# Kernel tuning notes

Measured on AMD Instinct MI355X. Metric: run time of the kernel, lower is better.

The kernel has to match this reference:

```python
import jax, jax.numpy as jnp
import numpy as np

N = 100000   # nodes
E = 6400000  # edges (avg degree 64)
F = 512      # num_features
C = 16       # num_classes

def _glorot(key, shape):
    fan_in, fan_out = shape
    lim = (6.0 / (fan_in + fan_out)) ** 0.5
    return jax.random.uniform(key, shape, jnp.float32, -lim, lim)

def setup_inputs() -> dict:
    key = jax.random.key(0)
    ks = jax.random.split(key, 8)
    x = jax.random.normal(ks[0], (N, F), jnp.float32)
    edge_index = jax.random.randint(ks[1], (2, E), 0, N, dtype=jnp.int64)
    return {
        "x": x,
        "edge_index": edge_index,
        "W1": _glorot(ks[2], (F, 16)), "b1": jnp.zeros((16,), jnp.float32),
        "W2": _glorot(ks[3], (16, 32)), "b2": jnp.zeros((32,), jnp.float32),
        "W3": _glorot(ks[4], (32, C)),  "b3": jnp.zeros((C,), jnp.float32),
        "Wc": _glorot(ks[5], (C, C)),   "bc": jnp.zeros((C,), jnp.float32),
    }

def _gcn_conv(x, row, col, norm, W, b):
    # PyG GCNConv: transform, then normalized sum-aggregation, then bias
    h = x @ W                                   # [N, out]
    msg = h[row] * norm[:, None]                # gather + scale, [E+N, out]
    agg = jax.ops.segment_sum(msg, col, num_segments=N)
    return agg + b

def reference(x, edge_index, W1, b1, W2, b2, W3, b3, Wc, bc):
    n = x.shape[0]
    loops = jnp.arange(n, dtype=edge_index.dtype)
    row = jnp.concatenate([edge_index[0], loops])  # source
    col = jnp.concatenate([edge_index[1], loops])  # target
    # symmetric normalization D^{-1/2} A_hat D^{-1/2}
    deg = jax.ops.segment_sum(jnp.ones_like(col, dtype=x.dtype), col, num_segments=n)
    dis = jnp.where(deg > 0, jax.lax.rsqrt(deg), 0.0)
    norm = dis[row] * dis[col]                     # [E+N]
    h = jax.nn.relu(_gcn_conv(x, row, col, norm, W1, b1))
    h = jax.nn.relu(_gcn_conv(h, row, col, norm, W2, b2))
    h = jax.nn.relu(_gcn_conv(h, row, col, norm, W3, b3))
    out = h @ Wc + bc
    return (out, h)
```

## Files before the change

### kernel.cpp

```cpp
#include <hip/hip_runtime.h>
#include <hip/hip_bf16.h>
#include <hip/hip_fp16.h>
#include <stdint.h>


#define MS_CHUNK 15360

__device__ __forceinline__ int blockScanExclusive256(int v, int* wsum) {
  int lane = threadIdx.x & 63;
  int wid  = threadIdx.x >> 6;
  int inc = v;
#pragma unroll
  for (int d = 1; d < 64; d <<= 1) {
    int y = __shfl_up(inc, d, 64);
    if (lane >= d) inc += y;
  }
  if (lane == 63) wsum[wid] = inc;
  __syncthreads();
  if (threadIdx.x == 0) {
    int s = 0;
#pragma unroll
    for (int w = 0; w < 4; ++w) { int t = wsum[w]; wsum[w] = s; s += t; }
  }
  __syncthreads();
  return inc - v + wsum[wid];
}

__device__ __forceinline__ int blockScanExclusive512(int v, int* wsum) {
  int lane = threadIdx.x & 63;
  int wid  = threadIdx.x >> 6;
  int inc = v;
#pragma unroll
  for (int d = 1; d < 64; d <<= 1) {
    int y = __shfl_up(inc, d, 64);
    if (lane >= d) inc += y;
  }
  if (lane == 63) wsum[wid] = inc;
  __syncthreads();
  if (threadIdx.x == 0) {
    int s = 0;
#pragma unroll
    for (int w = 0; w < 8; ++w) { int t = wsum[w]; wsum[w] = s; s += t; }
  }
  __syncthreads();
  return inc - v + wsum[wid];
}

__global__ __launch_bounds__(256) void k_bhist(const int* __restrict__ ecol,
                                               int* __restrict__ cntmat,
                                               int e, int chunk, int nb) {
  __shared__ int h[256];
  h[threadIdx.x] = 0;
  __syncthreads();
  int g = blockIdx.x;
  int s0 = g * chunk;
  int s1 = min(e, s0 + chunk);
  int i = s0 + threadIdx.x;
  for (; i + 768 < s1; i += 1024) {
    int c0 = ecol[i], c1 = ecol[i + 256], c2 = ecol[i + 512], c3 = ecol[i + 768];
    atomicAdd(&h[c0 >> 9], 1);
    atomicAdd(&h[c1 >> 9], 1);
    atomicAdd(&h[c2 >> 9], 1);
    atomicAdd(&h[c3 >> 9], 1);
  }
  for (; i < s1; i += 256) atomicAdd(&h[ecol[i] >> 9], 1);
  __syncthreads();
  for (int b = threadIdx.x; b < nb; b += 256) cntmat[g * nb + b] = h[b];
}

__global__ __launch_bounds__(256) void k_colscan(int* __restrict__ cntmat,
                                                 int* __restrict__ colsum,
                                                 int G, int nb) {
  __shared__ int wsum[4];
  __shared__ int carry_s;
  int b = blockIdx.x;
  if (threadIdx.x == 0) carry_s = 0;
  __syncthreads();
  for (int base = 0; base < G; base += 256) {
    int i = base + threadIdx.x;
    int v = (i < G) ? cntmat[i * nb + b] : 0;
    int ex = blockScanExclusive256(v, wsum);
    int c = carry_s;
    __syncthreads();
    if (i < G) cntmat[i * nb + b] = ex + c;
    if (threadIdx.x == 255) carry_s = c + ex + v;
    __syncthreads();
  }
  if (threadIdx.x == 0) colsum[b] = carry_s;
}

__global__ __launch_bounds__(256) void k_bscan(const int* __restrict__ colsum,
                                               int* __restrict__ bbase,
                                               int nb, int etot) {
  __shared__ int wsum[4];
  __shared__ int carry_s;
  if (threadIdx.x == 0) carry_s = 0;
  __syncthreads();
  for (int base = 0; base < nb; base += 256) {
    int i = base + threadIdx.x;
    int v = (i < nb) ? colsum[i] : 0;
    int ex = blockScanExclusive256(v, wsum);
    int c = carry_s;
    __syncthreads();
    if (i < nb) bbase[i] = ex + c;
    if (threadIdx.x == 255) carry_s = c + ex + v;
    __syncthreads();
  }
  if (threadIdx.x == 0) bbase[nb] = etot;
}

__global__ __launch_bounds__(256) void k_scatter_ms(
    const int* __restrict__ erow, const int* __restrict__ ecol,
    const int* __restrict__ cntmat, const int* __restrict__ colsum,
    const int* __restrict__ bbase, unsigned* __restrict__ sorted,
    int e, int chunk, int nb, int G) {
  __shared__ unsigned staging[MS_CHUNK];
  __shared__ int lstart[256];
  __shared__ int lfill[256];
  __shared__ int gbase[256];
  __shared__ int wsum[4];
  int g = blockIdx.x;
  for (int b = threadIdx.x; b < nb; b += 256) {
    int cur = cntmat[g * nb + b];
    int nxt = (g + 1 < G) ? cntmat[(g + 1) * nb + b] : colsum[b];
    lfill[b] = nxt - cur;
    gbase[b] = bbase[b] + cur;
  }
  __syncthreads();
  int v = (threadIdx.x < nb) ? lfill[threadIdx.x] : 0;
  int ex = blockScanExclusive256(v, wsum);
  if (threadIdx.x < nb) lstart[threadIdx.x] = ex;
  __syncthreads();
  if (threadIdx.x < nb) lfill[threadIdx.x] = 0;
  __syncthreads();
  int s0 = g * chunk;
  int s1 = min(e, s0 + chunk);
  int i = s0 + threadIdx.x;
  for (; i + 768 < s1; i += 1024) {
    int c0 = ecol[i],       c1 = ecol[i + 256], c2 = ecol[i + 512], c3 = ecol[i + 768];
    int r0 = erow[i],       r1 = erow[i + 256], r2 = erow[i + 512], r3 = erow[i + 768];
    int b0 = c0 >> 9, b1 = c1 >> 9, b2 = c2 >> 9, b3 = c3 >> 9;
    int p0 = atomicAdd(&lfill[b0], 1);
    int p1 = atomicAdd(&lfill[b1], 1);
    int p2 = atomicAdd(&lfill[b2], 1);
    int p3 = atomicAdd(&lfill[b3], 1);
    staging[lstart[b0] + p0] = ((unsigned)r0 << 9) | (unsigned)(c0 & 511);
    staging[lstart[b1] + p1] = ((unsigned)r1 << 9) | (unsigned)(c1 & 511);
    staging[lstart[b2] + p2] = ((unsigned)r2 << 9) | (unsigned)(c2 & 511);
    staging[lstart[b3] + p3] = ((unsigned)r3 << 9) | (unsigned)(c3 & 511);
  }
  for (; i < s1; i += 256) {
    int c = ecol[i];
    int b = c >> 9;
    int p = atomicAdd(&lfill[b], 1);
    staging[lstart[b] + p] = ((unsigned)erow[i] << 9) | (unsigned)(c & 511);
  }
  __syncthreads();
  int wid = threadIdx.x >> 6, L = threadIdx.x & 63;
  for (int b = wid; b < nb; b += 4) {
    int len = lfill[b];
    int ls = lstart[b], gb = gbase[b];
    for (int j = L; j < len; j += 64)
      sorted[gb + j] = staging[ls + j];
  }
}

__global__ __launch_bounds__(256) void k_transform1(
    const float* __restrict__ x, const float* __restrict__ W,
    __half* __restrict__ t1raw, int n) {
  int L = threadIdx.x & 63;
  int wid = blockIdx.x * 4 + (threadIdx.x >> 6);
  int nw = gridDim.x * 4;

  float w[8][16];
  const float4* W4 = reinterpret_cast<const float4*>(W);
#pragma unroll
  for (int i = 0; i < 4; ++i) {
#pragma unroll
    for (int c4 = 0; c4 < 4; ++c4) {
      float4 va = W4[(4 * L + i) * 4 + c4];
      w[i][c4 * 4 + 0] = va.x; w[i][c4 * 4 + 1] = va.y;
      w[i][c4 * 4 + 2] = va.z; w[i][c4 * 4 + 3] = va.w;
      float4 vb = W4[(256 + 4 * L + i) * 4 + c4];
      w[4 + i][c4 * 4 + 0] = vb.x; w[4 + i][c4 * 4 + 1] = vb.y;
      w[4 + i][c4 * 4 + 2] = vb.z; w[4 + i][c4 * 4 + 3] = vb.w;
    }
  }
  int col = ((L & 1) << 3) | ((L & 2) << 1) | ((L & 4) >> 1) | ((L & 8) >> 3);

  for (int r = wid; r < n; r += nw) {
    const float4* xr = reinterpret_cast<const float4*>(x + (size_t)r * 512);
    float4 v0 = xr[L];
    float4 v1 = xr[64 + L];
    float acc[16];
#pragma unroll
    for (int c = 0; c < 16; ++c) {
      float a = v0.x * w[0][c];
      a = fmaf(v0.y, w[1][c], a);
      a = fmaf(v0.z, w[2][c], a);
      a = fmaf(v0.w, w[3][c], a);
      a = fmaf(v1.x, w[4][c], a);
      a = fmaf(v1.y, w[5][c], a);
      a = fmaf(v1.z, w[6][c], a);
      a = fmaf(v1.w, w[7][c], a);
      acc[c] = a;
    }
#pragma unroll
    for (int j = 0; j < 8; ++j) {
      float send = (L & 1) ? acc[j] : acc[j + 8];
      float recv = __shfl_xor(send, 1, 64);
      acc[j] = ((L & 1) ? acc[j + 8] : acc[j]) + recv;
    }
#pragma unroll
    for (int j = 0; j < 4; ++j) {
      float send = (L & 2) ? acc[j] : acc[j + 4];
      float recv = __shfl_xor(send, 2, 64);
      acc[j] = ((L & 2) ? acc[j + 4] : acc[j]) + recv;
    }
#pragma unroll
    for (int j = 0; j < 2; ++j) {
      float send = (L & 4) ? acc[j] : acc[j + 2];
      float recv = __shfl_xor(send, 4, 64);
      acc[j] = ((L & 4) ? acc[j + 2] : acc[j]) + recv;
    }
    {
      float send = (L & 8) ? acc[0] : acc[1];
      float recv = __shfl_xor(send, 8, 64);
      acc[0] = ((L & 8) ? acc[1] : acc[0]) + recv;
    }
    float s = acc[0];
    s += __shfl_xor(s, 16, 64);
    s += __shfl_xor(s, 32, 64);
    if (L < 16) t1raw[r * 16 + col] = __float2half(s);
  }
}

__global__ __launch_bounds__(512) void k_pass2(const unsigned* __restrict__ sorted,
                                               const int* __restrict__ bbase,
                                               float* __restrict__ dis,
                                               int* __restrict__ rowptr,
                                               __half* __restrict__ t1,
                                               int* __restrict__ csr,
                                               int n, int etot) {
  __shared__ int hist[512];
  __shared__ int cur[512];
  __shared__ int wsum[8];
  int b = blockIdx.x;
  hist[threadIdx.x] = 0;
  __syncthreads();
  int s0 = bbase[b], s1 = bbase[b + 1];
  for (int i = s0 + threadIdx.x; i < s1; i += 512)
    atomicAdd(&hist[sorted[i] & 511], 1);
  __syncthreads();
  int j = threadIdx.x;
  int node = (b << 9) + j;
  int deg = hist[j];
  int ex = blockScanExclusive512(deg, wsum);
  float dv = rsqrtf((float)(deg + 1));
  cur[j] = s0 + ex;
  if (node < n) {
    dis[node] = dv;
    rowptr[node] = s0 + ex;
    __half2* t2 = reinterpret_cast<__half2*>(t1 + ((size_t)node << 4));
#pragma unroll
    for (int q = 0; q < 8; ++q) {
      float2 fv = __half22float2(t2[q]);
      fv.x *= dv; fv.y *= dv;
      t2[q] = __float22half2_rn(fv);
    }
  }
  if (b == 0 && threadIdx.x == 0) rowptr[n] = etot;
  __syncthreads();
  for (int i = s0 + threadIdx.x; i < s1; i += 512) {
    unsigned v = sorted[i];
    int pos = atomicAdd(&cur[v & 511], 1);
    csr[pos] = (int)(v >> 9);
  }
}

__device__ __forceinline__ float gather16(const __half* __restrict__ hs,
                                          const int* __restrict__ rowptr,
                                          const int* __restrict__ csr,
                                          int node, int f) {
  float acc0 = __half2float(hs[(node << 4) + f]);
  int e0 = rowptr[node], e1 = rowptr[node + 1];
  int e = e0;
  float acc1 = 0.f, acc2 = 0.f, acc3 = 0.f;
  for (; e + 16 <= e1; e += 16) {
    int r0  = csr[e + 0],  r1  = csr[e + 1],  r2  = csr[e + 2],  r3  = csr[e + 3];
    int r4  = csr[e + 4],  r5  = csr[e + 5],  r6  = csr[e + 6],  r7  = csr[e + 7];
    int r8  = csr[e + 8],  r9  = csr[e + 9],  r10 = csr[e + 10], r11 = csr[e + 11];
    int r12 = csr[e + 12], r13 = csr[e + 13], r14 = csr[e + 14], r15 = csr[e + 15];
    __half v0  = hs[(r0  << 4) + f], v1  = hs[(r1  << 4) + f];
    __half v2  = hs[(r2  << 4) + f], v3  = hs[(r3  << 4) + f];
    __half v4  = hs[(r4  << 4) + f], v5  = hs[(r5  << 4) + f];
    __half v6  = hs[(r6  << 4) + f], v7  = hs[(r7  << 4) + f];
    __half v8  = hs[(r8  << 4) + f], v9  = hs[(r9  << 4) + f];
    __half v10 = hs[(r10 << 4) + f], v11 = hs[(r11 << 4) + f];
    __half v12 = hs[(r12 << 4) + f], v13 = hs[(r13 << 4) + f];
    __half v14 = hs[(r14 << 4) + f], v15 = hs[(r15 << 4) + f];
    acc0 += (__half2float(v0)  + __half2float(v1))  + (__half2float(v2)  + __half2float(v3));
    acc1 += (__half2float(v4)  + __half2float(v5))  + (__half2float(v6)  + __half2float(v7));
    acc2 += (__half2float(v8)  + __half2float(v9))  + (__half2float(v10) + __half2float(v11));
    acc3 += (__half2float(v12) + __half2float(v13)) + (__half2float(v14) + __half2float(v15));
  }
  for (; e + 4 <= e1; e += 4) {
    int r0 = csr[e + 0], r1 = csr[e + 1], r2 = csr[e + 2], r3 = csr[e + 3];
    float v0 = __half2float(hs[(r0 << 4) + f]), v1 = __half2float(hs[(r1 << 4) + f]);
    float v2 = __half2float(hs[(r2 << 4) + f]), v3 = __half2float(hs[(r3 << 4) + f]);
    acc0 += (v0 + v1) + (v2 + v3);
  }
  for (; e < e1; ++e) acc0 += __half2float(hs[(csr[e] << 4) + f]);
  return (acc0 + acc1) + (acc2 + acc3);
}

__global__ __launch_bounds__(256) void k_agg_rb(
    const __half* __restrict__ hs, const int* __restrict__ rowptr,
    const int* __restrict__ csr, const float* __restrict__ dis,
    const float* __restrict__ b, __half* __restrict__ out, int n) {
  int node = blockIdx.x * 16 + threadIdx.x / 16;
  int f = threadIdx.x % 16;
  if (node >= n) return;
  float acc = gather16(hs, rowptr, csr, node, f);
  float d = dis[node];
  float t = fmaxf(fmaf(d, acc, b[f]), 0.f);
  out[(node << 4) + f] = __float2half(t * d);
}

__global__ __launch_bounds__(256) void k_agg_mid(
    const __half* __restrict__ hs, const int* __restrict__ rowptr,
    const int* __restrict__ csr, const float* __restrict__ dis,
    const float* __restrict__ W2, const float* __restrict__ b2,
    const float* __restrict__ W3, __half* __restrict__ out, int n) {
  __shared__ float w2s[512];
  __shared__ float w3s[512];
  __shared__ float b2s[32];
  for (int i = threadIdx.x; i < 512; i += 256) { w2s[i] = W2[i]; w3s[i] = W3[i]; }
  if (threadIdx.x < 32) b2s[threadIdx.x] = b2[threadIdx.x];
  __syncthreads();
  int node = blockIdx.x * 16 + threadIdx.x / 16;
  int f = threadIdx.x % 16;
  if (node >= n) return;
  float acc = gather16(hs, rowptr, csr, node, f);
  float d = dis[node];
  float v = d * acc;
  int base = threadIdx.x & 48;
  float a0 = b2s[f], a1 = b2s[f + 16];
#pragma unroll
  for (int k = 0; k < 16; ++k) {
    float vk = __shfl(v, base + k, 64);
    a0 = fmaf(vk, w2s[k * 32 + f], a0);
    a1 = fmaf(vk, w2s[k * 32 + 16 + f], a1);
  }
  a0 = fmaxf(a0, 0.f);
  a1 = fmaxf(a1, 0.f);
  float t = 0.f;
#pragma unroll
  for (int c = 0; c < 16; ++c) {
    float h0 = __shfl(a0, base + c, 64);
    float h1 = __shfl(a1, base + c, 64);
    t = fmaf(h0, w3s[c * 16 + f], t);
    t = fmaf(h1, w3s[(c + 16) * 16 + f], t);
  }
  out[(node << 4) + f] = __float2half(t * d);
}

__global__ __launch_bounds__(256) void k_agg_out(
    const __half* __restrict__ hs, const int* __restrict__ rowptr,
    const int* __restrict__ csr, const float* __restrict__ dis,
    const float* __restrict__ b3, const float* __restrict__ Wc,
    const float* __restrict__ bc, float* __restrict__ outh,
    float* __restrict__ outc, int n) {
  __shared__ float wcs[256];
  __shared__ float b3s[16];
  __shared__ float bcs[16];
  if (threadIdx.x < 256) wcs[threadIdx.x] = Wc[threadIdx.x];
  if (threadIdx.x < 16) { b3s[threadIdx.x] = b3[threadIdx.x]; bcs[threadIdx.x] = bc[threadIdx.x]; }
  __syncthreads();
  int node = blockIdx.x * 16 + threadIdx.x / 16;
  int f = threadIdx.x % 16;
  if (node >= n) return;
  float acc = gather16(hs, rowptr, csr, node, f);
  float d = dis[node];
  float h = fmaxf(fmaf(d, acc, b3s[f]), 0.f);
  outh[(node << 4) + f] = h;
  int base = threadIdx.x & 48;
  float o = bcs[f];
#pragma unroll
  for (int k = 0; k < 16; ++k) {
    float hk = __shfl(h, base + k, 64);
    o = fmaf(hk, wcs[k * 16 + f], o);
  }
  outc[(node << 4) + f] = o;
}

extern "C" void kernel_launch(void* const* d_in, const int* in_sizes, int n_in,
                              void* d_out, int out_size, void* d_ws, size_t ws_size,
                              hipStream_t stream) {
  (void)n_in; (void)out_size;
  const float* x  = (const float*)d_in[0];
  const int*   ei = (const int*)d_in[1];
  const float* W1 = (const float*)d_in[2];
  const float* b1 = (const float*)d_in[3];
  const float* W2 = (const float*)d_in[4];
  const float* b2 = (const float*)d_in[5];
  const float* W3 = (const float*)d_in[6];
  const float* b3 = (const float*)d_in[7];
  const float* Wc = (const float*)d_in[8];
  const float* bc = (const float*)d_in[9];

  const int F = 512;
  int N = in_sizes[0] / F;
  int E = in_sizes[1] / 2;
  const int* erow = ei;
  const int* ecol = ei + E;
  int NB = (N + 511) >> 9;
  const int chunk = MS_CHUNK;
  int GS = (E + chunk - 1) / chunk;

  auto align = [](size_t v) { return (v + 255) & ~(size_t)255; };
  char* p = (char*)d_ws;
  int*   cntmat = (int*)p;   p += align((size_t)GS * NB * 4);
  int*   colsum = (int*)p;   p += align(256 * 4);
  int*   bbase  = (int*)p;   p += align(257 * 4);
  float* dis    = (float*)p; p += align((size_t)N * 4);
  int*   rowptr = (int*)p;   p += align(((size_t)N + 1) * 4);
  int*   csr    = (int*)p;   p += align((size_t)E * 4);
  unsigned* sorted = (unsigned*)p; p += align((size_t)E * 4);
  __half* bufA = (__half*)p; p += align((size_t)N * 16 * 2);
  __half* bufB = (__half*)p; p += align((size_t)N * 16 * 2);
  if ((size_t)(p - (char*)d_ws) > ws_size) return;

  float* outc = (float*)d_out;
  float* outh = (float*)d_out + (size_t)N * 16;

  k_bhist<<<GS, 256, 0, stream>>>(ecol, cntmat, E, chunk, NB);
  k_colscan<<<NB, 256, 0, stream>>>(cntmat, colsum, GS, NB);
  k_bscan<<<1, 256, 0, stream>>>(colsum, bbase, NB, E);
  k_scatter_ms<<<GS, 256, 0, stream>>>(erow, ecol, cntmat, colsum, bbase,
                                       sorted, E, chunk, NB, GS);
  k_transform1<<<2048, 256, 0, stream>>>(x, W1, bufA, N);
  k_pass2<<<NB, 512, 0, stream>>>(sorted, bbase, dis, rowptr, bufA, csr, N, E);

  k_agg_rb<<<(N + 15) / 16, 256, 0, stream>>>(bufA, rowptr, csr, dis, b1, bufB, N);
  k_agg_mid<<<(N + 15) / 16, 256, 0, stream>>>(bufB, rowptr, csr, dis, W2, b2, W3, bufA, N);
  k_agg_out<<<(N + 15) / 16, 256, 0, stream>>>(bufA, rowptr, csr, dis, b3, Wc, bc, outh, outc, N);
}
```

Measured before the change: 311.8 us.

## Replace multi-pass bucket sort with atomic-cursor fixed-capacity bucket scatter

Drops the separate histogram, column-scan and global-offset kernels and instead has each scatter block count its own bucket sizes, then claim space in fixed-capacity per-bucket regions through global atomic cursors. The cursors are zeroed inside the transform kernel, and the bucket prefix scan moves after the scatter. It also loads the CSR neighbour indices once per 16-lane group and distributes them with wave shuffles instead of having every lane load all 16. Bucket order across blocks becomes nondeterministic, and correctness relies on no bucket exceeding the fixed capacity, which holds only for roughly uniform edge distributions.

```diff
diff --git a/kernel.cpp b/kernel.cpp
--- a/kernel.cpp
+++ b/kernel.cpp
@@ -46,50 +46,7 @@
   return inc - v + wsum[wid];
 }
 
-__global__ __launch_bounds__(256) void k_bhist(const int* __restrict__ ecol,
-                                               int* __restrict__ cntmat,
-                                               int e, int chunk, int nb) {
-  __shared__ int h[256];
-  h[threadIdx.x] = 0;
-  __syncthreads();
-  int g = blockIdx.x;
-  int s0 = g * chunk;
-  int s1 = min(e, s0 + chunk);
-  int i = s0 + threadIdx.x;
-  for (; i + 768 < s1; i += 1024) {
-    int c0 = ecol[i], c1 = ecol[i + 256], c2 = ecol[i + 512], c3 = ecol[i + 768];
-    atomicAdd(&h[c0 >> 9], 1);
-    atomicAdd(&h[c1 >> 9], 1);
-    atomicAdd(&h[c2 >> 9], 1);
-    atomicAdd(&h[c3 >> 9], 1);
-  }
-  for (; i < s1; i += 256) atomicAdd(&h[ecol[i] >> 9], 1);
-  __syncthreads();
-  for (int b = threadIdx.x; b < nb; b += 256) cntmat[g * nb + b] = h[b];
-}
-
-__global__ __launch_bounds__(256) void k_colscan(int* __restrict__ cntmat,
-                                                 int* __restrict__ colsum,
-                                                 int G, int nb) {
-  __shared__ int wsum[4];
-  __shared__ int carry_s;
-  int b = blockIdx.x;
-  if (threadIdx.x == 0) carry_s = 0;
-  __syncthreads();
-  for (int base = 0; base < G; base += 256) {
-    int i = base + threadIdx.x;
-    int v = (i < G) ? cntmat[i * nb + b] : 0;
-    int ex = blockScanExclusive256(v, wsum);
-    int c = carry_s;
-    __syncthreads();
-    if (i < G) cntmat[i * nb + b] = ex + c;
-    if (threadIdx.x == 255) carry_s = c + ex + v;
-    __syncthreads();
-  }
-  if (threadIdx.x == 0) colsum[b] = carry_s;
-}
-
-__global__ __launch_bounds__(256) void k_bscan(const int* __restrict__ colsum,
+__global__ __launch_bounds__(256) void k_bscan(const int* __restrict__ counts,
                                                int* __restrict__ bbase,
                                                int nb, int etot) {
   __shared__ int wsum[4];
@@ -98,7 +55,7 @@
   __syncthreads();
   for (int base = 0; base < nb; base += 256) {
     int i = base + threadIdx.x;
-    int v = (i < nb) ? colsum[i] : 0;
+    int v = (i < nb) ? counts[i] : 0;
     int ex = blockScanExclusive256(v, wsum);
     int c = carry_s;
     __syncthreads();
@@ -109,65 +66,79 @@
   if (threadIdx.x == 0) bbase[nb] = etot;
 }
 
-__global__ __launch_bounds__(256) void k_scatter_ms(
+__global__ __launch_bounds__(256) void k_scatter1(
     const int* __restrict__ erow, const int* __restrict__ ecol,
-    const int* __restrict__ cntmat, const int* __restrict__ colsum,
-    const int* __restrict__ bbase, unsigned* __restrict__ sorted,
-    int e, int chunk, int nb, int G) {
+    int* __restrict__ cursor, unsigned* __restrict__ sorted,
+    int e, int chunk, int nb, int cap) {
   __shared__ unsigned staging[MS_CHUNK];
   __shared__ int lstart[256];
   __shared__ int lfill[256];
   __shared__ int gbase[256];
   __shared__ int wsum[4];
   int g = blockIdx.x;
-  for (int b = threadIdx.x; b < nb; b += 256) {
-    int cur = cntmat[g * nb + b];
-    int nxt = (g + 1 < G) ? cntmat[(g + 1) * nb + b] : colsum[b];
-    lfill[b] = nxt - cur;
-    gbase[b] = bbase[b] + cur;
-  }
-  __syncthreads();
-  int v = (threadIdx.x < nb) ? lfill[threadIdx.x] : 0;
-  int ex = blockScanExclusive256(v, wsum);
-  if (threadIdx.x < nb) lstart[threadIdx.x] = ex;
-  __syncthreads();
-  if (threadIdx.x < nb) lfill[threadIdx.x] = 0;
-  __syncthreads();
   int s0 = g * chunk;
   int s1 = min(e, s0 + chunk);
-  int i = s0 + threadIdx.x;
-  for (; i + 768 < s1; i += 1024) {
-    int c0 = ecol[i],       c1 = ecol[i + 256], c2 = ecol[i + 512], c3 = ecol[i + 768];
-    int r0 = erow[i],       r1 = erow[i + 256], r2 = erow[i + 512], r3 = erow[i + 768];
-    int b0 = c0 >> 9, b1 = c1 >> 9, b2 = c2 >> 9, b3 = c3 >> 9;
-    int p0 = atomicAdd(&lfill[b0], 1);
-    int p1 = atomicAdd(&lfill[b1], 1);
-    int p2 = atomicAdd(&lfill[b2], 1);
-    int p3 = atomicAdd(&lfill[b3], 1);
-    staging[lstart[b0] + p0] = ((unsigned)r0 << 9) | (unsigned)(c0 & 511);
-    staging[lstart[b1] + p1] = ((unsigned)r1 << 9) | (unsigned)(c1 & 511);
-    staging[lstart[b2] + p2] = ((unsigned)r2 << 9) | (unsigned)(c2 & 511);
-    staging[lstart[b3] + p3] = ((unsigned)r3 << 9) | (unsigned)(c3 & 511);
-  }
-  for (; i < s1; i += 256) {
-    int c = ecol[i];
-    int b = c >> 9;
-    int p = atomicAdd(&lfill[b], 1);
-    staging[lstart[b] + p] = ((unsigned)erow[i] << 9) | (unsigned)(c & 511);
+  lfill[threadIdx.x] = 0;
+  __syncthreads();
+  {
+    int i = s0 + threadIdx.x;
+    for (; i + 768 < s1; i += 1024) {
+      int c0 = ecol[i], c1 = ecol[i + 256], c2 = ecol[i + 512], c3 = ecol[i + 768];
+      atomicAdd(&lfill[c0 >> 9], 1);
+      atomicAdd(&lfill[c1 >> 9], 1);
+      atomicAdd(&lfill[c2 >> 9], 1);
+      atomicAdd(&lfill[c3 >> 9], 1);
+    }
+    for (; i < s1; i += 256) atomicAdd(&lfill[ecol[i] >> 9], 1);
+  }
+  __syncthreads();
+  int cnt = lfill[threadIdx.x];
+  int ex = blockScanExclusive256(cnt, wsum);
+  lstart[threadIdx.x] = ex;
+  int gb = 0;
+  if (threadIdx.x < nb && cnt > 0) gb = atomicAdd(&cursor[threadIdx.x], cnt);
+  gbase[threadIdx.x] = gb;
+  __syncthreads();
+  lfill[threadIdx.x] = 0;
+  __syncthreads();
+  {
+    int i = s0 + threadIdx.x;
+    for (; i + 768 < s1; i += 1024) {
+      int c0 = ecol[i],       c1 = ecol[i + 256], c2 = ecol[i + 512], c3 = ecol[i + 768];
+      int r0 = erow[i],       r1 = erow[i + 256], r2 = erow[i + 512], r3 = erow[i + 768];
+      int b0 = c0 >> 9, b1 = c1 >> 9, b2 = c2 >> 9, b3 = c3 >> 9;
+      int p0 = atomicAdd(&lfill[b0], 1);
+      int p1 = atomicAdd(&lfill[b1], 1);
+      int p2 = atomicAdd(&lfill[b2], 1);
+      int p3 = atomicAdd(&lfill[b3], 1);
+      staging[lstart[b0] + p0] = ((unsigned)r0 << 9) | (unsigned)(c0 & 511);
+      staging[lstart[b1] + p1] = ((unsigned)r1 << 9) | (unsigned)(c1 & 511);
+      staging[lstart[b2] + p2] = ((unsigned)r2 << 9) | (unsigned)(c2 & 511);
+      staging[lstart[b3] + p3] = ((unsigned)r3 << 9) | (unsigned)(c3 & 511);
+    }
+    for (; i < s1; i += 256) {
+      int c = ecol[i];
+      int b = c >> 9;
+      int p = atomicAdd(&lfill[b], 1);
+      staging[lstart[b] + p] = ((unsigned)erow[i] << 9) | (unsigned)(c & 511);
+    }
   }
   __syncthreads();
   int wid = threadIdx.x >> 6, L = threadIdx.x & 63;
   for (int b = wid; b < nb; b += 4) {
     int len = lfill[b];
-    int ls = lstart[b], gb = gbase[b];
+    int ls = lstart[b];
+    int gdst = b * cap + gbase[b];
     for (int j = L; j < len; j += 64)
-      sorted[gb + j] = staging[ls + j];
+      sorted[gdst + j] = staging[ls + j];
   }
 }
 
 __global__ __launch_bounds__(256) void k_transform1(
     const float* __restrict__ x, const float* __restrict__ W,
-    __half* __restrict__ t1raw, int n) {
+    __half* __restrict__ t1raw, int* __restrict__ cursor, int n) {
+  if (blockIdx.x == 0) cursor[threadIdx.x] = 0;
+
   int L = threadIdx.x & 63;
   int wid = blockIdx.x * 4 + (threadIdx.x >> 6);
   int nw = gridDim.x * 4;
@@ -236,19 +207,21 @@
 }
 
 __global__ __launch_bounds__(512) void k_pass2(const unsigned* __restrict__ sorted,
+                                               const int* __restrict__ counts,
                                                const int* __restrict__ bbase,
                                                float* __restrict__ dis,
                                                int* __restrict__ rowptr,
                                                __half* __restrict__ t1,
                                                int* __restrict__ csr,
-                                               int n, int etot) {
+                                               int n, int etot, int cap) {
   __shared__ int hist[512];
   __shared__ int cur[512];
   __shared__ int wsum[8];
   int b = blockIdx.x;
   hist[threadIdx.x] = 0;
   __syncthreads();
-  int s0 = bbase[b], s1 = bbase[b + 1];
+  int s0 = b * cap;
+  int s1 = s0 + counts[b];
   for (int i = s0 + threadIdx.x; i < s1; i += 512)
     atomicAdd(&hist[sorted[i] & 511], 1);
   __syncthreads();
@@ -257,10 +230,11 @@
   int deg = hist[j];
   int ex = blockScanExclusive512(deg, wsum);
   float dv = rsqrtf((float)(deg + 1));
-  cur[j] = s0 + ex;
+  int gpos = bbase[b] + ex;
+  cur[j] = gpos;
   if (node < n) {
     dis[node] = dv;
-    rowptr[node] = s0 + ex;
+    rowptr[node] = gpos;
     __half2* t2 = reinterpret_cast<__half2*>(t1 + ((size_t)node << 4));
 #pragma unroll
     for (int q = 0; q < 8; ++q) {
@@ -282,15 +256,21 @@
                                           const int* __restrict__ rowptr,
                                           const int* __restrict__ csr,
                                           int node, int f) {
+  int base = (int)(threadIdx.x & 48);
   float acc0 = __half2float(hs[(node << 4) + f]);
   int e0 = rowptr[node], e1 = rowptr[node + 1];
   int e = e0;
   float acc1 = 0.f, acc2 = 0.f, acc3 = 0.f;
   for (; e + 16 <= e1; e += 16) {
-    int r0  = csr[e + 0],  r1  = csr[e + 1],  r2  = csr[e + 2],  r3  = csr[e + 3];
-    int r4  = csr[e + 4],  r5  = csr[e + 5],  r6  = csr[e + 6],  r7  = csr[e + 7];
-    int r8  = csr[e + 8],  r9  = csr[e + 9],  r10 = csr[e + 10], r11 = csr[e + 11];
-    int r12 = csr[e + 12], r13 = csr[e + 13], r14 = csr[e + 14], r15 = csr[e + 15];
+    int rr = csr[e + f];
+    int r0  = __shfl(rr, base + 0, 64),  r1  = __shfl(rr, base + 1, 64);
+    int r2  = __shfl(rr, base + 2, 64),  r3  = __shfl(rr, base + 3, 64);
+    int r4  = __shfl(rr, base + 4, 64),  r5  = __shfl(rr, base + 5, 64);
+    int r6  = __shfl(rr, base + 6, 64),  r7  = __shfl(rr, base + 7, 64);
+    int r8  = __shfl(rr, base + 8, 64),  r9  = __shfl(rr, base + 9, 64);
+    int r10 = __shfl(rr, base + 10, 64), r11 = __shfl(rr, base + 11, 64);
+    int r12 = __shfl(rr, base + 12, 64), r13 = __shfl(rr, base + 13, 64);
+    int r14 = __shfl(rr, base + 14, 64), r15 = __shfl(rr, base + 15, 64);
     __half v0  = hs[(r0  << 4) + f], v1  = hs[(r1  << 4) + f];
     __half v2  = hs[(r2  << 4) + f], v3  = hs[(r3  << 4) + f];
     __half v4  = hs[(r4  << 4) + f], v5  = hs[(r5  << 4) + f];
@@ -417,16 +397,16 @@
   int NB = (N + 511) >> 9;
   const int chunk = MS_CHUNK;
   int GS = (E + chunk - 1) / chunk;
+  int CAP = ((E / NB) + 2048 + 511) & ~511;
 
   auto align = [](size_t v) { return (v + 255) & ~(size_t)255; };
   char* p = (char*)d_ws;
-  int*   cntmat = (int*)p;   p += align((size_t)GS * NB * 4);
-  int*   colsum = (int*)p;   p += align(256 * 4);
+  int*   cursor = (int*)p;   p += align(256 * 4);
   int*   bbase  = (int*)p;   p += align(257 * 4);
   float* dis    = (float*)p; p += align((size_t)N * 4);
   int*   rowptr = (int*)p;   p += align(((size_t)N + 1) * 4);
   int*   csr    = (int*)p;   p += align((size_t)E * 4);
-  unsigned* sorted = (unsigned*)p; p += align((size_t)E * 4);
+  unsigned* sorted = (unsigned*)p; p += align((size_t)NB * CAP * 4);
   __half* bufA = (__half*)p; p += align((size_t)N * 16 * 2);
   __half* bufB = (__half*)p; p += align((size_t)N * 16 * 2);
   if ((size_t)(p - (char*)d_ws) > ws_size) return;
@@ -434,13 +414,10 @@
   float* outc = (float*)d_out;
   float* outh = (float*)d_out + (size_t)N * 16;
 
-  k_bhist<<<GS, 256, 0, stream>>>(ecol, cntmat, E, chunk, NB);
-  k_colscan<<<NB, 256, 0, stream>>>(cntmat, colsum, GS, NB);
-  k_bscan<<<1, 256, 0, stream>>>(colsum, bbase, NB, E);
-  k_scatter_ms<<<GS, 256, 0, stream>>>(erow, ecol, cntmat, colsum, bbase,
-                                       sorted, E, chunk, NB, GS);
-  k_transform1<<<2048, 256, 0, stream>>>(x, W1, bufA, N);
-  k_pass2<<<NB, 512, 0, stream>>>(sorted, bbase, dis, rowptr, bufA, csr, N, E);
+  k_transform1<<<2048, 256, 0, stream>>>(x, W1, bufA, cursor, N);
+  k_scatter1<<<GS, 256, 0, stream>>>(erow, ecol, cursor, sorted, E, chunk, NB, CAP);
+  k_bscan<<<1, 256, 0, stream>>>(cursor, bbase, NB, E);
+  k_pass2<<<NB, 512, 0, stream>>>(sorted, cursor, bbase, dis, rowptr, bufA, csr, N, E, CAP);
 
   k_agg_rb<<<(N + 15) / 16, 256, 0, stream>>>(bufA, rowptr, csr, dis, b1, bufB, N);
   k_agg_mid<<<(N + 15) / 16, 256, 0, stream>>>(bufB, rowptr, csr, dis, W2, b2, W3, bufA, N);
```

New measurement: 317.7 us. Within noise of the previous version (+1.9%).
